# Performance work log

Measured on AMD Instinct MI355X. Metric: run time of the kernel, lower is better.

Reference implementation:

```python
import jax, jax.numpy as jnp
import numpy as np

LN_EPS = 1e-5


def setup_inputs() -> dict:
    key = jax.random.key(0)
    ks = jax.random.split(key, 8)
    B, S, N, D, H, E = 8, 32, 2048, 64, 128, 32768
    x_sequence = jax.random.normal(ks[0], (B, S, N, D), dtype=jnp.float32)
    edge_index = jax.random.randint(ks[1], (2, E), 0, N, dtype=jnp.int64)
    batch = jax.random.randint(ks[2], (B * N,), 0, B, dtype=jnp.int64)
    scale = 0.05
    Wz = jax.random.normal(ks[3], (D + H, H), dtype=jnp.float32) * scale
    Wr = jax.random.normal(ks[4], (D + H, H), dtype=jnp.float32) * scale
    Wc = jax.random.normal(ks[5], (D + H, H), dtype=jnp.float32) * scale
    bz = jnp.zeros((H,), jnp.float32)
    br = jnp.zeros((H,), jnp.float32)
    bc = jnp.zeros((H,), jnp.float32)
    ln_gamma = jnp.ones((H,), jnp.float32)
    ln_beta = jnp.zeros((H,), jnp.float32)
    return dict(x_sequence=x_sequence, edge_index=edge_index, batch=batch,
                Wz=Wz, bz=bz, Wr=Wr, br=br, Wc=Wc, bc=bc,
                ln_gamma=ln_gamma, ln_beta=ln_beta)


def reference(x_sequence, edge_index, batch, Wz, bz, Wr, br, Wc, bc, ln_gamma, ln_beta):
    B, S, N, D = x_sequence.shape
    H = Wz.shape[1]
    NT = B * N

    # Batch the per-graph edge list by offsetting node ids per batch element.
    offsets = jnp.arange(B, dtype=edge_index.dtype) * N
    src = (edge_index[0][None, :] + offsets[:, None]).reshape(-1)
    dst = (edge_index[1][None, :] + offsets[:, None]).reshape(-1)
    # GCNConv: add self loops, symmetric normalization D^-1/2 (A+I) D^-1/2.
    loops = jnp.arange(NT, dtype=edge_index.dtype)
    src = jnp.concatenate([src, loops])
    dst = jnp.concatenate([dst, loops])
    deg = jax.ops.segment_sum(jnp.ones_like(src, x_sequence.dtype), dst, num_segments=NT)
    dinv = jnp.where(deg > 0, jax.lax.rsqrt(jnp.maximum(deg, 1e-12)), 0.0)
    norm = dinv[src] * dinv[dst]  # [E_total]

    def gcn(x, W, b):
        h = x @ W                                   # [NT, H]
        msg = h[src] * norm[:, None]                # gather + scale
        return jax.ops.segment_sum(msg, dst, num_segments=NT) + b

    def layer_norm(h):
        mu = jnp.mean(h, axis=-1, keepdims=True)
        var = jnp.mean(jnp.square(h - mu), axis=-1, keepdims=True)
        return (h - mu) * jax.lax.rsqrt(var + LN_EPS) * ln_gamma + ln_beta

    def step(h_prev, x_t):
        # x_t: [NT, D], h_prev: [NT, H]
        xh = jnp.concatenate([x_t, h_prev], axis=1)
        z = jax.nn.sigmoid(gcn(xh, Wz, bz))
        r = jax.nn.sigmoid(gcn(xh, Wr, br))
        xrh = jnp.concatenate([x_t, r * h_prev], axis=1)
        cand = jnp.tanh(gcn(xrh, Wc, bc))
        h_new = layer_norm((1.0 - z) * h_prev + z * cand)
        return h_new, None

    xs = x_sequence.transpose(1, 0, 2, 3).reshape(S, NT, D)
    h0 = jnp.zeros((NT, H), x_sequence.dtype)
    h_final, _ = jax.lax.scan(step, h0, xs)

    # global_mean_pool over nodes per batch element (contiguous blocks of N).
    pooled = h_final.reshape(B, N, H).mean(axis=1)
    return pooled
```

## Files before the change

kernel.cpp:

```cpp
#include <hip/hip_runtime.h>
#include <math.h>

#define NB 8
#define NS 32
#define NN 2048
#define ND 64
#define NH 128
#define NE 32768
#define NT (NB*NN)
#define LN_EPS 1e-5f

typedef __attribute__((ext_vector_type(8))) short short8v;
typedef __attribute__((ext_vector_type(4))) float f32x4;
typedef __attribute__((ext_vector_type(4))) unsigned int u32x4;

static __device__ inline unsigned short f2bf(float f) {
  union { float f; unsigned int u; } v; v.f = f;
  unsigned int r = v.u + 0x7fffu + ((v.u >> 16) & 1u);
  return (unsigned short)(r >> 16);
}

static __device__ inline void bf8_to_f(const unsigned short* __restrict__ p, float* f) {
  u32x4 v = *(const u32x4*)p;
#pragma unroll
  for (int i = 0; i < 4; i++) {
    union { unsigned int u; float x; } lo, hi;
    lo.u = v[i] << 16; hi.u = v[i] & 0xFFFF0000u;
    f[2*i] = lo.x; f[2*i+1] = hi.x;
  }
}


__global__ void k_count(const int* __restrict__ dst, int* __restrict__ deg) {
  int e = blockIdx.x * blockDim.x + threadIdx.x;
  if (e < NE) atomicAdd(&deg[dst[e]], 1);
}

__global__ void k_scan(const int* __restrict__ deg, int* __restrict__ row_start,
                       float* __restrict__ dinv) {
  if (threadIdx.x == 0) {
    int acc = 0;
    for (int n = 0; n < NN; n++) { row_start[n] = acc; acc += deg[n]; }
    row_start[NN] = acc;
  }
  for (int n = threadIdx.x; n < NN; n += blockDim.x) {
    dinv[n] = rsqrtf((float)(deg[n] + 1));
  }
}

__global__ void k_scatter(const int* __restrict__ src, const int* __restrict__ dst,
                          const int* __restrict__ row_start, int* __restrict__ cursor,
                          int* __restrict__ csr_src) {
  int e = blockIdx.x * blockDim.x + threadIdx.x;
  if (e < NE) {
    int d = dst[e];
    int pos = atomicAdd(&cursor[d], 1);
    csr_src[row_start[d] + pos] = src[e];
  }
}


__global__ void k_wcvt(const float* __restrict__ Wz, const float* __restrict__ Wr,
                       const float* __restrict__ Wc,
                       unsigned short* __restrict__ Wt_zr, unsigned short* __restrict__ Wt_c) {
  int col = blockIdx.x;
  int k = threadIdx.x;
  float v = (col < 128) ? Wz[k * 128 + col] : Wr[k * 128 + (col - 128)];
  Wt_zr[(size_t)col * 192 + k] = f2bf(v);
  if (col < 128) Wt_c[(size_t)col * 192 + k] = f2bf(Wc[k * 128 + col]);
}


__global__ __launch_bounds__(256)
void k_xT(const float* __restrict__ x, unsigned short* __restrict__ xT) {
  int blk = blockIdx.x;
  int s = blk >> 9;
  int n0 = (blk & 511) * 4;
  int t = threadIdx.x;
  int b = t >> 5;
  int d2 = (t & 31) * 2;
#pragma unroll
  for (int i = 0; i < 4; i++) {
    int n = n0 + i;
    const float2 v = *(const float2*)(x + (((size_t)b * NS + s) * NN + n) * ND + d2);
    unsigned int p = ((unsigned int)f2bf(v.y) << 16) | f2bf(v.x);
    *(unsigned int*)(xT + (((size_t)s * NN + n) * NB + b) * ND + d2) = p;
  }
}


__global__ __launch_bounds__(256)
void k_aggX2(const unsigned short* __restrict__ xT, const int* __restrict__ row_start,
             const int* __restrict__ csr_src, const float* __restrict__ dinv,
             unsigned short* __restrict__ Xa) {
  int bid = blockIdx.x;
  int bs = (bid & 7) * 2048 + (bid >> 3);
  int rid = bs * 4 + (threadIdx.x >> 6);
  int lane = threadIdx.x & 63;
  int s = rid >> 11, n = rid & 2047;
  const unsigned short* xs = xT + (size_t)s * (NN * NB * ND);
  float dn = dinv[n];
  float acc[8], val[8];
  bf8_to_f(xs + (size_t)n * 512 + lane * 8, val);
#pragma unroll
  for (int i = 0; i < 8; i++) acc[i] = dn * val[i];
  int k0 = row_start[n], k1 = row_start[n + 1];
  for (int kb = k0; kb < k1; kb += 64) {
    int m = k1 - kb; if (m > 64) m = 64;
    int idx = 0; float wv = 0.f;
    if (lane < m) { idx = csr_src[kb + lane]; wv = dinv[idx]; }
    for (int k = 0; k < m; k++) {
      int sn = __shfl(idx, k, 64);
      float ww = __shfl(wv, k, 64);
      bf8_to_f(xs + (size_t)sn * 512 + lane * 8, val);
#pragma unroll
      for (int i = 0; i < 8; i++) acc[i] = fmaf(ww, val[i], acc[i]);
    }
  }
  unsigned int pk[4];
#pragma unroll
  for (int i = 0; i < 4; i++)
    pk[i] = ((unsigned int)f2bf(dn * acc[2*i+1]) << 16) | f2bf(dn * acc[2*i]);
  *(u32x4*)(Xa + (size_t)rid * 512 + lane * 8) = *(u32x4*)pk;
}


__global__ __launch_bounds__(256)
void k_zrF(const unsigned short* __restrict__ Xa, const unsigned short* __restrict__ hB,
           const float* __restrict__ h, const unsigned short* __restrict__ Wt,
           const int* __restrict__ row_start, const int* __restrict__ csr_src,
           const float* __restrict__ dinv,
           const float* __restrict__ bz, const float* __restrict__ br,
           float* __restrict__ z, unsigned short* __restrict__ rhB, int s) {
  __shared__ unsigned short ha[16 * 128];
  int tid = threadIdx.x;
  int lane = tid & 63;
  int w = tid >> 6;
  int n0 = blockIdx.x * 2;
  int j = w >> 1, half = w & 1;
  int n = n0 + j;
  float dn = dinv[n];
  float acc[8], val[8];
  int foff = half * 512 + lane * 8;
  bf8_to_f(hB + (size_t)n * (NB * NH) + foff, val);
#pragma unroll
  for (int i = 0; i < 8; i++) acc[i] = dn * val[i];
  int k0 = row_start[n], k1 = row_start[n + 1];
  for (int kb = k0; kb < k1; kb += 64) {
    int m = k1 - kb; if (m > 64) m = 64;
    int idx = 0; float wv = 0.f;
    if (lane < m) { idx = csr_src[kb + lane]; wv = dinv[idx]; }
    for (int k = 0; k < m; k++) {
      int sn = __shfl(idx, k, 64);
      float ww = __shfl(wv, k, 64);
      bf8_to_f(hB + (size_t)sn * (NB * NH) + foff, val);
#pragma unroll
      for (int i = 0; i < 8; i++) acc[i] = fmaf(ww, val[i], acc[i]);
    }
  }
  {
    int row = j * 8 + (foff >> 7);
    int f = foff & 127;
    unsigned int pk[4];
#pragma unroll
    for (int i = 0; i < 4; i++)
      pk[i] = ((unsigned int)f2bf(dn * acc[2*i+1]) << 16) | f2bf(dn * acc[2*i]);
    int byte = (row * 256 + f * 2) ^ ((row & 7) << 4);
    *(u32x4*)((char*)ha + byte) = *(u32x4*)pk;
  }
  __syncthreads();
  int ar = lane & 15;
  int koff = (lane >> 4) * 8;
  short8v afr[6];
  const unsigned short* xrow =
      Xa + (((size_t)s * NN + n0 + (ar >> 3)) * NB + (ar & 7)) * ND;
  afr[0] = *(const short8v*)(xrow + koff);
  afr[1] = *(const short8v*)(xrow + 32 + koff);
#pragma unroll
  for (int kb = 2; kb < 6; kb++) {
    int kk = (kb - 2) * 32 + koff;
    int byte = (ar * 256 + kk * 2) ^ ((ar & 7) << 4);
    afr[kb] = *(const short8v*)((char*)ha + byte);
  }
  f32x4 cacc[4];
#pragma unroll
  for (int ct = 0; ct < 4; ct++) cacc[ct] = (f32x4){0.f, 0.f, 0.f, 0.f};
#pragma unroll
  for (int ct = 0; ct < 4; ct++) {
    const unsigned short* wcol = Wt + (size_t)((w * 4 + ct) * 16 + (lane & 15)) * 192;
#pragma unroll
    for (int kb = 0; kb < 6; kb++) {
      short8v bfr = *(const short8v*)(wcol + kb * 32 + koff);
      cacc[ct] = __builtin_amdgcn_mfma_f32_16x16x32_bf16(afr[kb], bfr, cacc[ct], 0, 0, 0);
    }
  }
  int r0 = (lane >> 4) * 4;
#pragma unroll
  for (int ct = 0; ct < 4; ct++) {
    int col = (w * 4 + ct) * 16 + (lane & 15);
    int isz = (col < 128);
    int f = isz ? col : col - 128;
    float bias = isz ? bz[f] : br[f];
#pragma unroll
    for (int q = 0; q < 4; q++) {
      int r = r0 + q;
      size_t gidx = (((size_t)(n0 + (r >> 3))) * NB + (r & 7)) * NH + f;
      float g = cacc[ct][q] + bias;
      float sg = 1.f / (1.f + __expf(-g));
      if (isz) z[gidx] = sg;
      else rhB[gidx] = f2bf(sg * h[gidx]);
    }
  }
}


__global__ __launch_bounds__(256)
void k_cF(const unsigned short* __restrict__ Xa, const unsigned short* __restrict__ rhB,
          const float* __restrict__ z, const unsigned short* __restrict__ Wt,
          const int* __restrict__ row_start, const int* __restrict__ csr_src,
          const float* __restrict__ dinv, const float* __restrict__ bc,
          const float* __restrict__ gamma, const float* __restrict__ beta,
          float* __restrict__ h, unsigned short* __restrict__ hB, int s) {
  __shared__ unsigned short rha[16 * 128];
  __shared__ float lsum[4][16], lsq[4][16];
  int tid = threadIdx.x;
  int lane = tid & 63;
  int w = tid >> 6;
  int n0 = blockIdx.x * 2;
  int j = w >> 1, half = w & 1;
  int n = n0 + j;
  float dn = dinv[n];
  float acc[8], val[8];
  int foff = half * 512 + lane * 8;
  bf8_to_f(rhB + (size_t)n * (NB * NH) + foff, val);
#pragma unroll
  for (int i = 0; i < 8; i++) acc[i] = dn * val[i];
  int k0 = row_start[n], k1 = row_start[n + 1];
  for (int kb = k0; kb < k1; kb += 64) {
    int m = k1 - kb; if (m > 64) m = 64;
    int idx = 0; float wv = 0.f;
    if (lane < m) { idx = csr_src[kb + lane]; wv = dinv[idx]; }
    for (int k = 0; k < m; k++) {
      int sn = __shfl(idx, k, 64);
      float ww = __shfl(wv, k, 64);
      bf8_to_f(rhB + (size_t)sn * (NB * NH) + foff, val);
#pragma unroll
      for (int i = 0; i < 8; i++) acc[i] = fmaf(ww, val[i], acc[i]);
    }
  }
  {
    int row = j * 8 + (foff >> 7);
    int f = foff & 127;
    unsigned int pk[4];
#pragma unroll
    for (int i = 0; i < 4; i++)
      pk[i] = ((unsigned int)f2bf(dn * acc[2*i+1]) << 16) | f2bf(dn * acc[2*i]);
    int byte = (row * 256 + f * 2) ^ ((row & 7) << 4);
    *(u32x4*)((char*)rha + byte) = *(u32x4*)pk;
  }
  __syncthreads();
  int ar = lane & 15;
  int koff = (lane >> 4) * 8;
  short8v afr[6];
  const unsigned short* xrow =
      Xa + (((size_t)s * NN + n0 + (ar >> 3)) * NB + (ar & 7)) * ND;
  afr[0] = *(const short8v*)(xrow + koff);
  afr[1] = *(const short8v*)(xrow + 32 + koff);
#pragma unroll
  for (int kb = 2; kb < 6; kb++) {
    int kk = (kb - 2) * 32 + koff;
    int byte = (ar * 256 + kk * 2) ^ ((ar & 7) << 4);
    afr[kb] = *(const short8v*)((char*)rha + byte);
  }
  f32x4 cacc[2];
  cacc[0] = (f32x4){0.f, 0.f, 0.f, 0.f};
  cacc[1] = (f32x4){0.f, 0.f, 0.f, 0.f};
#pragma unroll
  for (int ct = 0; ct < 2; ct++) {
    const unsigned short* wcol = Wt + (size_t)((w * 2 + ct) * 16 + (lane & 15)) * 192;
#pragma unroll
    for (int kb = 0; kb < 6; kb++) {
      short8v bfr = *(const short8v*)(wcol + kb * 32 + koff);
      cacc[ct] = __builtin_amdgcn_mfma_f32_16x16x32_bf16(afr[kb], bfr, cacc[ct], 0, 0, 0);
    }
  }
  int r0 = (lane >> 4) * 4;
  float u[2][4];
  float psum[4] = {0.f, 0.f, 0.f, 0.f};
  float psq[4] = {0.f, 0.f, 0.f, 0.f};
#pragma unroll
  for (int ct = 0; ct < 2; ct++) {
    int col = (w * 2 + ct) * 16 + (lane & 15);
    float bcc = bc[col];
#pragma unroll
    for (int q = 0; q < 4; q++) {
      int r = r0 + q;
      size_t gidx = (((size_t)(n0 + (r >> 3))) * NB + (r & 7)) * NH + col;
      float gc = cacc[ct][q] + bcc;
      float ea = __expf(-2.f * fabsf(gc));
      float th = (1.f - ea) / (1.f + ea);
      float cand = copysignf(th, gc);
      float zv = z[gidx];
      float uu = (1.f - zv) * h[gidx] + zv * cand;
      u[ct][q] = uu;
      psum[q] += uu; psq[q] += uu * uu;
    }
  }
#pragma unroll
  for (int q = 0; q < 4; q++) {
    float s1 = psum[q], s2 = psq[q];
#pragma unroll
    for (int o = 1; o <= 8; o <<= 1) {
      s1 += __shfl_xor(s1, o, 64);
      s2 += __shfl_xor(s2, o, 64);
    }
    if ((lane & 15) == 0) {
      lsum[w][r0 + q] = s1; lsq[w][r0 + q] = s2;
    }
  }
  __syncthreads();
#pragma unroll
  for (int ct = 0; ct < 2; ct++) {
    int col = (w * 2 + ct) * 16 + (lane & 15);
    float g = gamma[col], bt = beta[col];
#pragma unroll
    for (int q = 0; q < 4; q++) {
      int r = r0 + q;
      float tot = lsum[0][r] + lsum[1][r] + lsum[2][r] + lsum[3][r];
      float totq = lsq[0][r] + lsq[1][r] + lsq[2][r] + lsq[3][r];
      float mu = tot * (1.f / NH);
      float var = totq * (1.f / NH) - mu * mu;
      float inv = rsqrtf(var + LN_EPS);
      float hv = (u[ct][q] - mu) * inv * g + bt;
      size_t gidx = (((size_t)(n0 + (r >> 3))) * NB + (r & 7)) * NH + col;
      h[gidx] = hv;
      hB[gidx] = f2bf(hv);
    }
  }
}


__global__ __launch_bounds__(128)
void k_pool(const float* __restrict__ h, float* __restrict__ out) {
  int b = blockIdx.x & 7;
  int c = blockIdx.x >> 3;
  int f = threadIdx.x;
  float acc = 0.f;
  for (int n = c * 128; n < c * 128 + 128; n++)
    acc += h[((size_t)n * NB + b) * NH + f];
  atomicAdd(&out[b * NH + f], acc * (1.f / NN));
}


extern "C" void kernel_launch(void* const* d_in, const int* in_sizes, int n_in,
                              void* d_out, int out_size, void* d_ws, size_t ws_size,
                              hipStream_t stream) {
  const float* x     = (const float*)d_in[0];
  const int*   ei    = (const int*)d_in[1];
  const float* Wz    = (const float*)d_in[3];
  const float* bz    = (const float*)d_in[4];
  const float* Wr    = (const float*)d_in[5];
  const float* br    = (const float*)d_in[6];
  const float* Wc    = (const float*)d_in[7];
  const float* bc    = (const float*)d_in[8];
  const float* gamma = (const float*)d_in[9];
  const float* beta  = (const float*)d_in[10];
  float* out = (float*)d_out;

  char* ws = (char*)d_ws;
  size_t off = 0;
  auto alloc = [&](size_t bytes) {
    void* p = ws + off;
    off = (off + bytes + 255) & ~(size_t)255;
    return p;
  };
  float* h  = (float*)alloc((size_t)NT * NH * 4);
  float* z  = (float*)alloc((size_t)NT * NH * 4);
  unsigned short* hB   = (unsigned short*)alloc((size_t)NT * NH * 2);
  unsigned short* rhB  = (unsigned short*)alloc((size_t)NT * NH * 2);
  unsigned short* xT   = (unsigned short*)alloc((size_t)NS * NN * NB * ND * 2);
  unsigned short* Xa   = (unsigned short*)alloc((size_t)NS * NN * NB * ND * 2);
  unsigned short* Wt_zr = (unsigned short*)alloc((size_t)256 * 192 * 2);
  unsigned short* Wt_c  = (unsigned short*)alloc((size_t)128 * 192 * 2);
  float* dinv = (float*)alloc(NN * 4);
  int* deg       = (int*)alloc(NN * 4);
  int* row_start = (int*)alloc((NN + 1) * 4);
  int* cursor    = (int*)alloc(NN * 4);
  int* csr_src   = (int*)alloc(NE * 4);

  const int* e_src = ei;
  const int* e_dst = ei + NE;

  hipMemsetAsync(h, 0, (size_t)NT * NH * 4, stream);
  hipMemsetAsync(hB, 0, (size_t)NT * NH * 2, stream);
  hipMemsetAsync(deg, 0, NN * 4, stream);
  hipMemsetAsync(cursor, 0, NN * 4, stream);
  hipMemsetAsync(d_out, 0, (size_t)NB * NH * 4, stream);

  k_count<<<NE / 256, 256, 0, stream>>>(e_dst, deg);
  k_scan<<<1, 256, 0, stream>>>(deg, row_start, dinv);
  k_scatter<<<NE / 256, 256, 0, stream>>>(e_src, e_dst, row_start, cursor, csr_src);
  k_wcvt<<<256, 192, 0, stream>>>(Wz, Wr, Wc, Wt_zr, Wt_c);
  k_xT<<<16384, 256, 0, stream>>>(x, xT);
  k_aggX2<<<16384, 256, 0, stream>>>(xT, row_start, csr_src, dinv, Xa);

  for (int s = 0; s < NS; s++) {
    k_zrF<<<NN / 2, 256, 0, stream>>>(Xa, hB, h, Wt_zr, row_start, csr_src, dinv,
                                      bz, br, z, rhB, s);
    k_cF<<<NN / 2, 256, 0, stream>>>(Xa, rhB, z, Wt_c, row_start, csr_src, dinv,
                                     bc, gamma, beta, h, hB, s);
  }
  k_pool<<<128, 128, 0, stream>>>(h, out);
}
```

Baseline: 1.783 ms.

## Drop fp32 hidden state, store z as fp16, double threads per step block

The fp32 hidden state and fp32 z buffers are removed. The recurrence now keeps only the bf16 hidden state, and z is stored in fp16, which roughly halves per-step global traffic. Both per-step kernels go from 256 to 512 threads, so each wave gathers 4 features instead of 8 and owns fewer MFMA output tiles, and the edge loops are unrolled by 4. The cost is precision: hidden state is carried in bf16 across all 32 steps, so rounding error can build up.

```diff
diff --git a/kernel.cpp b/kernel.cpp
--- a/kernel.cpp
+++ b/kernel.cpp
@@ -13,17 +13,31 @@
 typedef __attribute__((ext_vector_type(8))) short short8v;
 typedef __attribute__((ext_vector_type(4))) float f32x4;
 typedef __attribute__((ext_vector_type(4))) unsigned int u32x4;
+typedef __attribute__((ext_vector_type(2))) unsigned int u32x2;
 
 static __device__ inline unsigned short f2bf(float f) {
   union { float f; unsigned int u; } v; v.f = f;
   unsigned int r = v.u + 0x7fffu + ((v.u >> 16) & 1u);
   return (unsigned short)(r >> 16);
 }
+static __device__ inline float bf2f(unsigned short s) {
+  union { unsigned int u; float f; } v; v.u = ((unsigned int)s) << 16;
+  return v.f;
+}
 
 static __device__ inline void bf8_to_f(const unsigned short* __restrict__ p, float* f) {
   u32x4 v = *(const u32x4*)p;
 #pragma unroll
   for (int i = 0; i < 4; i++) {
+    union { unsigned int u; float x; } lo, hi;
+    lo.u = v[i] << 16; hi.u = v[i] & 0xFFFF0000u;
+    f[2*i] = lo.x; f[2*i+1] = hi.x;
+  }
+}
+static __device__ inline void bf4_to_f(const unsigned short* __restrict__ p, float* f) {
+  u32x2 v = *(const u32x2*)p;
+#pragma unroll
+  for (int i = 0; i < 2; i++) {
     union { unsigned int u; float x; } lo, hi;
     lo.u = v[i] << 16; hi.u = v[i] & 0xFFFF0000u;
     f[2*i] = lo.x; f[2*i+1] = hi.x;
@@ -109,6 +123,7 @@
     int m = k1 - kb; if (m > 64) m = 64;
     int idx = 0; float wv = 0.f;
     if (lane < m) { idx = csr_src[kb + lane]; wv = dinv[idx]; }
+#pragma unroll 4
     for (int k = 0; k < m; k++) {
       int sn = __shfl(idx, k, 64);
       float ww = __shfl(wv, k, 64);
@@ -125,48 +140,49 @@
 }
 
 
-__global__ __launch_bounds__(256)
+__global__ __launch_bounds__(512, 8)
 void k_zrF(const unsigned short* __restrict__ Xa, const unsigned short* __restrict__ hB,
-           const float* __restrict__ h, const unsigned short* __restrict__ Wt,
+           const unsigned short* __restrict__ Wt,
            const int* __restrict__ row_start, const int* __restrict__ csr_src,
            const float* __restrict__ dinv,
            const float* __restrict__ bz, const float* __restrict__ br,
-           float* __restrict__ z, unsigned short* __restrict__ rhB, int s) {
+           _Float16* __restrict__ zH, unsigned short* __restrict__ rhB, int s) {
   __shared__ unsigned short ha[16 * 128];
   int tid = threadIdx.x;
   int lane = tid & 63;
   int w = tid >> 6;
   int n0 = blockIdx.x * 2;
-  int j = w >> 1, half = w & 1;
+  int j = w >> 2, q = w & 3;
   int n = n0 + j;
   float dn = dinv[n];
-  float acc[8], val[8];
-  int foff = half * 512 + lane * 8;
-  bf8_to_f(hB + (size_t)n * (NB * NH) + foff, val);
-#pragma unroll
-  for (int i = 0; i < 8; i++) acc[i] = dn * val[i];
+  float acc[4], val[4];
+  int foff = q * 256 + lane * 4;
+  bf4_to_f(hB + (size_t)n * (NB * NH) + foff, val);
+#pragma unroll
+  for (int i = 0; i < 4; i++) acc[i] = dn * val[i];
   int k0 = row_start[n], k1 = row_start[n + 1];
   for (int kb = k0; kb < k1; kb += 64) {
     int m = k1 - kb; if (m > 64) m = 64;
     int idx = 0; float wv = 0.f;
     if (lane < m) { idx = csr_src[kb + lane]; wv = dinv[idx]; }
+#pragma unroll 4
     for (int k = 0; k < m; k++) {
       int sn = __shfl(idx, k, 64);
       float ww = __shfl(wv, k, 64);
-      bf8_to_f(hB + (size_t)sn * (NB * NH) + foff, val);
-#pragma unroll
-      for (int i = 0; i < 8; i++) acc[i] = fmaf(ww, val[i], acc[i]);
+      bf4_to_f(hB + (size_t)sn * (NB * NH) + foff, val);
+#pragma unroll
+      for (int i = 0; i < 4; i++) acc[i] = fmaf(ww, val[i], acc[i]);
     }
   }
   {
     int row = j * 8 + (foff >> 7);
-    int f = foff & 127;
-    unsigned int pk[4];
-#pragma unroll
-    for (int i = 0; i < 4; i++)
+    int fe = foff & 127;
+    unsigned int pk[2];
+#pragma unroll
+    for (int i = 0; i < 2; i++)
       pk[i] = ((unsigned int)f2bf(dn * acc[2*i+1]) << 16) | f2bf(dn * acc[2*i]);
-    int byte = (row * 256 + f * 2) ^ ((row & 7) << 4);
-    *(u32x4*)((char*)ha + byte) = *(u32x4*)pk;
+    int byte = (row * 256 + fe * 2) ^ ((row & 7) << 4);
+    *(u32x2*)((char*)ha + byte) = *(u32x2*)pk;
   }
   __syncthreads();
   int ar = lane & 15;
@@ -182,12 +198,12 @@
     int byte = (ar * 256 + kk * 2) ^ ((ar & 7) << 4);
     afr[kb] = *(const short8v*)((char*)ha + byte);
   }
-  f32x4 cacc[4];
-#pragma unroll
-  for (int ct = 0; ct < 4; ct++) cacc[ct] = (f32x4){0.f, 0.f, 0.f, 0.f};
-#pragma unroll
-  for (int ct = 0; ct < 4; ct++) {
-    const unsigned short* wcol = Wt + (size_t)((w * 4 + ct) * 16 + (lane & 15)) * 192;
+  f32x4 cacc[2];
+  cacc[0] = (f32x4){0.f, 0.f, 0.f, 0.f};
+  cacc[1] = (f32x4){0.f, 0.f, 0.f, 0.f};
+#pragma unroll
+  for (int ct = 0; ct < 2; ct++) {
+    const unsigned short* wcol = Wt + (size_t)((2 * w + ct) * 16 + (lane & 15)) * 192;
 #pragma unroll
     for (int kb = 0; kb < 6; kb++) {
       short8v bfr = *(const short8v*)(wcol + kb * 32 + koff);
@@ -196,67 +212,68 @@
   }
   int r0 = (lane >> 4) * 4;
 #pragma unroll
-  for (int ct = 0; ct < 4; ct++) {
-    int col = (w * 4 + ct) * 16 + (lane & 15);
+  for (int ct = 0; ct < 2; ct++) {
+    int col = (2 * w + ct) * 16 + (lane & 15);
     int isz = (col < 128);
     int f = isz ? col : col - 128;
     float bias = isz ? bz[f] : br[f];
 #pragma unroll
-    for (int q = 0; q < 4; q++) {
-      int r = r0 + q;
+    for (int qq = 0; qq < 4; qq++) {
+      int r = r0 + qq;
       size_t gidx = (((size_t)(n0 + (r >> 3))) * NB + (r & 7)) * NH + f;
-      float g = cacc[ct][q] + bias;
+      float g = cacc[ct][qq] + bias;
       float sg = 1.f / (1.f + __expf(-g));
-      if (isz) z[gidx] = sg;
-      else rhB[gidx] = f2bf(sg * h[gidx]);
-    }
-  }
-}
-
-
-__global__ __launch_bounds__(256)
+      if (isz) zH[gidx] = (_Float16)sg;
+      else rhB[gidx] = f2bf(sg * bf2f(hB[gidx]));
+    }
+  }
+}
+
+
+__global__ __launch_bounds__(512, 8)
 void k_cF(const unsigned short* __restrict__ Xa, const unsigned short* __restrict__ rhB,
-          const float* __restrict__ z, const unsigned short* __restrict__ Wt,
+          const _Float16* __restrict__ zH, const unsigned short* __restrict__ Wt,
           const int* __restrict__ row_start, const int* __restrict__ csr_src,
           const float* __restrict__ dinv, const float* __restrict__ bc,
           const float* __restrict__ gamma, const float* __restrict__ beta,
-          float* __restrict__ h, unsigned short* __restrict__ hB, int s) {
+          unsigned short* __restrict__ hB, int s) {
   __shared__ unsigned short rha[16 * 128];
-  __shared__ float lsum[4][16], lsq[4][16];
+  __shared__ float lsum[8][16], lsq[8][16];
   int tid = threadIdx.x;
   int lane = tid & 63;
   int w = tid >> 6;
   int n0 = blockIdx.x * 2;
-  int j = w >> 1, half = w & 1;
+  int j = w >> 2, q = w & 3;
   int n = n0 + j;
   float dn = dinv[n];
-  float acc[8], val[8];
-  int foff = half * 512 + lane * 8;
-  bf8_to_f(rhB + (size_t)n * (NB * NH) + foff, val);
-#pragma unroll
-  for (int i = 0; i < 8; i++) acc[i] = dn * val[i];
+  float acc[4], val[4];
+  int foff = q * 256 + lane * 4;
+  bf4_to_f(rhB + (size_t)n * (NB * NH) + foff, val);
+#pragma unroll
+  for (int i = 0; i < 4; i++) acc[i] = dn * val[i];
   int k0 = row_start[n], k1 = row_start[n + 1];
   for (int kb = k0; kb < k1; kb += 64) {
     int m = k1 - kb; if (m > 64) m = 64;
     int idx = 0; float wv = 0.f;
     if (lane < m) { idx = csr_src[kb + lane]; wv = dinv[idx]; }
+#pragma unroll 4
     for (int k = 0; k < m; k++) {
       int sn = __shfl(idx, k, 64);
       float ww = __shfl(wv, k, 64);
-      bf8_to_f(rhB + (size_t)sn * (NB * NH) + foff, val);
-#pragma unroll
-      for (int i = 0; i < 8; i++) acc[i] = fmaf(ww, val[i], acc[i]);
+      bf4_to_f(rhB + (size_t)sn * (NB * NH) + foff, val);
+#pragma unroll
+      for (int i = 0; i < 4; i++) acc[i] = fmaf(ww, val[i], acc[i]);
     }
   }
   {
     int row = j * 8 + (foff >> 7);
-    int f = foff & 127;
-    unsigned int pk[4];
-#pragma unroll
-    for (int i = 0; i < 4; i++)
+    int fe = foff & 127;
+    unsigned int pk[2];
+#pragma unroll
+    for (int i = 0; i < 2; i++)
       pk[i] = ((unsigned int)f2bf(dn * acc[2*i+1]) << 16) | f2bf(dn * acc[2*i]);
-    int byte = (row * 256 + f * 2) ^ ((row & 7) << 4);
-    *(u32x4*)((char*)rha + byte) = *(u32x4*)pk;
+    int byte = (row * 256 + fe * 2) ^ ((row & 7) << 4);
+    *(u32x2*)((char*)rha + byte) = *(u32x2*)pk;
   }
   __syncthreads();
   int ar = lane & 15;
@@ -272,82 +289,70 @@
     int byte = (ar * 256 + kk * 2) ^ ((ar & 7) << 4);
     afr[kb] = *(const short8v*)((char*)rha + byte);
   }
-  f32x4 cacc[2];
-  cacc[0] = (f32x4){0.f, 0.f, 0.f, 0.f};
-  cacc[1] = (f32x4){0.f, 0.f, 0.f, 0.f};
-#pragma unroll
-  for (int ct = 0; ct < 2; ct++) {
-    const unsigned short* wcol = Wt + (size_t)((w * 2 + ct) * 16 + (lane & 15)) * 192;
+  f32x4 cacc = {0.f, 0.f, 0.f, 0.f};
+  {
+    const unsigned short* wcol = Wt + (size_t)(w * 16 + (lane & 15)) * 192;
 #pragma unroll
     for (int kb = 0; kb < 6; kb++) {
       short8v bfr = *(const short8v*)(wcol + kb * 32 + koff);
-      cacc[ct] = __builtin_amdgcn_mfma_f32_16x16x32_bf16(afr[kb], bfr, cacc[ct], 0, 0, 0);
+      cacc = __builtin_amdgcn_mfma_f32_16x16x32_bf16(afr[kb], bfr, cacc, 0, 0, 0);
     }
   }
   int r0 = (lane >> 4) * 4;
-  float u[2][4];
-  float psum[4] = {0.f, 0.f, 0.f, 0.f};
-  float psq[4] = {0.f, 0.f, 0.f, 0.f};
-#pragma unroll
-  for (int ct = 0; ct < 2; ct++) {
-    int col = (w * 2 + ct) * 16 + (lane & 15);
-    float bcc = bc[col];
-#pragma unroll
-    for (int q = 0; q < 4; q++) {
-      int r = r0 + q;
-      size_t gidx = (((size_t)(n0 + (r >> 3))) * NB + (r & 7)) * NH + col;
-      float gc = cacc[ct][q] + bcc;
-      float ea = __expf(-2.f * fabsf(gc));
-      float th = (1.f - ea) / (1.f + ea);
-      float cand = copysignf(th, gc);
-      float zv = z[gidx];
-      float uu = (1.f - zv) * h[gidx] + zv * cand;
-      u[ct][q] = uu;
-      psum[q] += uu; psq[q] += uu * uu;
-    }
-  }
-#pragma unroll
-  for (int q = 0; q < 4; q++) {
-    float s1 = psum[q], s2 = psq[q];
+  int col = w * 16 + (lane & 15);
+  float u[4];
+  float bcc = bc[col];
+#pragma unroll
+  for (int qq = 0; qq < 4; qq++) {
+    int r = r0 + qq;
+    size_t gidx = (((size_t)(n0 + (r >> 3))) * NB + (r & 7)) * NH + col;
+    float gc = cacc[qq] + bcc;
+    float ea = __expf(-2.f * fabsf(gc));
+    float th = (1.f - ea) / (1.f + ea);
+    float cand = copysignf(th, gc);
+    float zv = (float)zH[gidx];
+    float uu = (1.f - zv) * bf2f(hB[gidx]) + zv * cand;
+    u[qq] = uu;
+  }
+#pragma unroll
+  for (int qq = 0; qq < 4; qq++) {
+    float s1 = u[qq], s2 = u[qq] * u[qq];
 #pragma unroll
     for (int o = 1; o <= 8; o <<= 1) {
       s1 += __shfl_xor(s1, o, 64);
       s2 += __shfl_xor(s2, o, 64);
     }
     if ((lane & 15) == 0) {
-      lsum[w][r0 + q] = s1; lsq[w][r0 + q] = s2;
+      lsum[w][r0 + qq] = s1; lsq[w][r0 + qq] = s2;
     }
   }
   __syncthreads();
-#pragma unroll
-  for (int ct = 0; ct < 2; ct++) {
-    int col = (w * 2 + ct) * 16 + (lane & 15);
-    float g = gamma[col], bt = beta[col];
-#pragma unroll
-    for (int q = 0; q < 4; q++) {
-      int r = r0 + q;
-      float tot = lsum[0][r] + lsum[1][r] + lsum[2][r] + lsum[3][r];
-      float totq = lsq[0][r] + lsq[1][r] + lsq[2][r] + lsq[3][r];
-      float mu = tot * (1.f / NH);
-      float var = totq * (1.f / NH) - mu * mu;
-      float inv = rsqrtf(var + LN_EPS);
-      float hv = (u[ct][q] - mu) * inv * g + bt;
-      size_t gidx = (((size_t)(n0 + (r >> 3))) * NB + (r & 7)) * NH + col;
-      h[gidx] = hv;
-      hB[gidx] = f2bf(hv);
-    }
+  float g = gamma[col], bt = beta[col];
+#pragma unroll
+  for (int qq = 0; qq < 4; qq++) {
+    int r = r0 + qq;
+    float tot = lsum[0][r] + lsum[1][r] + lsum[2][r] + lsum[3][r]
+              + lsum[4][r] + lsum[5][r] + lsum[6][r] + lsum[7][r];
+    float totq = lsq[0][r] + lsq[1][r] + lsq[2][r] + lsq[3][r]
+               + lsq[4][r] + lsq[5][r] + lsq[6][r] + lsq[7][r];
+    float mu = tot * (1.f / NH);
+    float var = totq * (1.f / NH) - mu * mu;
+    float inv = rsqrtf(var + LN_EPS);
+    float hv = (u[qq] - mu) * inv * g + bt;
+    size_t gidx = (((size_t)(n0 + (r >> 3))) * NB + (r & 7)) * NH + col;
+    hB[gidx] = f2bf(hv);
   }
 }
 
 
 __global__ __launch_bounds__(128)
-void k_pool(const float* __restrict__ h, float* __restrict__ out) {
+void k_pool(const unsigned short* __restrict__ hB, float* __restrict__ out) {
   int b = blockIdx.x & 7;
   int c = blockIdx.x >> 3;
   int f = threadIdx.x;
   float acc = 0.f;
   for (int n = c * 128; n < c * 128 + 128; n++)
-    acc += h[((size_t)n * NB + b) * NH + f];
+    acc += bf2f(hB[((size_t)n * NB + b) * NH + f]);
   atomicAdd(&out[b * NH + f], acc * (1.f / NN));
 }
 
@@ -374,10 +379,9 @@
     off = (off + bytes + 255) & ~(size_t)255;
     return p;
   };
-  float* h  = (float*)alloc((size_t)NT * NH * 4);
-  float* z  = (float*)alloc((size_t)NT * NH * 4);
   unsigned short* hB   = (unsigned short*)alloc((size_t)NT * NH * 2);
   unsigned short* rhB  = (unsigned short*)alloc((size_t)NT * NH * 2);
+  _Float16*       zH   = (_Float16*)alloc((size_t)NT * NH * 2);
   unsigned short* xT   = (unsigned short*)alloc((size_t)NS * NN * NB * ND * 2);
   unsigned short* Xa   = (unsigned short*)alloc((size_t)NS * NN * NB * ND * 2);
   unsigned short* Wt_zr = (unsigned short*)alloc((size_t)256 * 192 * 2);
@@ -391,7 +395,6 @@
   const int* e_src = ei;
   const int* e_dst = ei + NE;
 
-  hipMemsetAsync(h, 0, (size_t)NT * NH * 4, stream);
   hipMemsetAsync(hB, 0, (size_t)NT * NH * 2, stream);
   hipMemsetAsync(deg, 0, NN * 4, stream);
   hipMemsetAsync(cursor, 0, NN * 4, stream);
@@ -405,10 +408,10 @@
   k_aggX2<<<16384, 256, 0, stream>>>(xT, row_start, csr_src, dinv, Xa);
 
   for (int s = 0; s < NS; s++) {
-    k_zrF<<<NN / 2, 256, 0, stream>>>(Xa, hB, h, Wt_zr, row_start, csr_src, dinv,
-                                      bz, br, z, rhB, s);
-    k_cF<<<NN / 2, 256, 0, stream>>>(Xa, rhB, z, Wt_c, row_start, csr_src, dinv,
-                                     bc, gamma, beta, h, hB, s);
-  }
-  k_pool<<<128, 128, 0, stream>>>(h, out);
-}
+    k_zrF<<<NN / 2, 512, 0, stream>>>(Xa, hB, Wt_zr, row_start, csr_src, dinv,
+                                      bz, br, zH, rhB, s);
+    k_cF<<<NN / 2, 512, 0, stream>>>(Xa, rhB, zH, Wt_c, row_start, csr_src, dinv,
+                                     bc, gamma, beta, hB, s);
+  }
+  k_pool<<<128, 128, 0, stream>>>(hB, out);
+}
```

New measurement: 1.814 ms. About the same (+1.7%).

## Drop fp32 hidden state, store z in fp16, scalarize CSR neighbor loops

Applied to the files above, without the earlier changes.

Removes the fp32 copies of the hidden state and update gate, keeping h only in bf16 and z in fp16, which cuts global memory traffic in the per-step recurrent kernels. The gather loops now read the neighbor index and weight through scalar-uniform loads (readfirstlane bounds) instead of lane-distributed loads plus shuffles, and are unrolled. Carrying the recurrent state in bf16 across 32 steps lowers its precision, and the result may drift from the reference.

```diff
diff --git a/kernel.cpp b/kernel.cpp
--- a/kernel.cpp
+++ b/kernel.cpp
@@ -13,11 +13,16 @@
 typedef __attribute__((ext_vector_type(8))) short short8v;
 typedef __attribute__((ext_vector_type(4))) float f32x4;
 typedef __attribute__((ext_vector_type(4))) unsigned int u32x4;
+typedef __attribute__((ext_vector_type(2))) unsigned int u32x2;
 
 static __device__ inline unsigned short f2bf(float f) {
   union { float f; unsigned int u; } v; v.f = f;
   unsigned int r = v.u + 0x7fffu + ((v.u >> 16) & 1u);
   return (unsigned short)(r >> 16);
+}
+static __device__ inline float bf2f(unsigned short s) {
+  union { unsigned int u; float f; } v; v.u = ((unsigned int)s) << 16;
+  return v.f;
 }
 
 static __device__ inline void bf8_to_f(const unsigned short* __restrict__ p, float* f) {
@@ -97,25 +102,23 @@
   int bs = (bid & 7) * 2048 + (bid >> 3);
   int rid = bs * 4 + (threadIdx.x >> 6);
   int lane = threadIdx.x & 63;
-  int s = rid >> 11, n = rid & 2047;
+  int s = rid >> 11;
+  int n = __builtin_amdgcn_readfirstlane(rid & 2047);
   const unsigned short* xs = xT + (size_t)s * (NN * NB * ND);
   float dn = dinv[n];
   float acc[8], val[8];
   bf8_to_f(xs + (size_t)n * 512 + lane * 8, val);
 #pragma unroll
   for (int i = 0; i < 8; i++) acc[i] = dn * val[i];
-  int k0 = row_start[n], k1 = row_start[n + 1];
-  for (int kb = k0; kb < k1; kb += 64) {
-    int m = k1 - kb; if (m > 64) m = 64;
-    int idx = 0; float wv = 0.f;
-    if (lane < m) { idx = csr_src[kb + lane]; wv = dinv[idx]; }
-    for (int k = 0; k < m; k++) {
-      int sn = __shfl(idx, k, 64);
-      float ww = __shfl(wv, k, 64);
-      bf8_to_f(xs + (size_t)sn * 512 + lane * 8, val);
-#pragma unroll
-      for (int i = 0; i < 8; i++) acc[i] = fmaf(ww, val[i], acc[i]);
-    }
+  int k0 = __builtin_amdgcn_readfirstlane(row_start[n]);
+  int k1 = __builtin_amdgcn_readfirstlane(row_start[n + 1]);
+#pragma unroll 4
+  for (int k = k0; k < k1; k++) {
+    int sn = csr_src[k];
+    float ww = dinv[sn];
+    bf8_to_f(xs + (size_t)sn * 512 + lane * 8, val);
+#pragma unroll
+    for (int i = 0; i < 8; i++) acc[i] = fmaf(ww, val[i], acc[i]);
   }
   unsigned int pk[4];
 #pragma unroll
@@ -127,45 +130,42 @@
 
 __global__ __launch_bounds__(256)
 void k_zrF(const unsigned short* __restrict__ Xa, const unsigned short* __restrict__ hB,
-           const float* __restrict__ h, const unsigned short* __restrict__ Wt,
+           const unsigned short* __restrict__ Wt,
            const int* __restrict__ row_start, const int* __restrict__ csr_src,
            const float* __restrict__ dinv,
            const float* __restrict__ bz, const float* __restrict__ br,
-           float* __restrict__ z, unsigned short* __restrict__ rhB, int s) {
+           _Float16* __restrict__ zH, unsigned short* __restrict__ rhB, int s) {
   __shared__ unsigned short ha[16 * 128];
   int tid = threadIdx.x;
   int lane = tid & 63;
   int w = tid >> 6;
   int n0 = blockIdx.x * 2;
   int j = w >> 1, half = w & 1;
-  int n = n0 + j;
+  int n = __builtin_amdgcn_readfirstlane(n0 + j);
   float dn = dinv[n];
   float acc[8], val[8];
   int foff = half * 512 + lane * 8;
   bf8_to_f(hB + (size_t)n * (NB * NH) + foff, val);
 #pragma unroll
   for (int i = 0; i < 8; i++) acc[i] = dn * val[i];
-  int k0 = row_start[n], k1 = row_start[n + 1];
-  for (int kb = k0; kb < k1; kb += 64) {
-    int m = k1 - kb; if (m > 64) m = 64;
-    int idx = 0; float wv = 0.f;
-    if (lane < m) { idx = csr_src[kb + lane]; wv = dinv[idx]; }
-    for (int k = 0; k < m; k++) {
-      int sn = __shfl(idx, k, 64);
-      float ww = __shfl(wv, k, 64);
-      bf8_to_f(hB + (size_t)sn * (NB * NH) + foff, val);
-#pragma unroll
-      for (int i = 0; i < 8; i++) acc[i] = fmaf(ww, val[i], acc[i]);
-    }
+  int k0 = __builtin_amdgcn_readfirstlane(row_start[n]);
+  int k1 = __builtin_amdgcn_readfirstlane(row_start[n + 1]);
+#pragma unroll 4
+  for (int k = k0; k < k1; k++) {
+    int sn = csr_src[k];
+    float ww = dinv[sn];
+    bf8_to_f(hB + (size_t)sn * (NB * NH) + foff, val);
+#pragma unroll
+    for (int i = 0; i < 8; i++) acc[i] = fmaf(ww, val[i], acc[i]);
   }
   {
     int row = j * 8 + (foff >> 7);
-    int f = foff & 127;
+    int fe = foff & 127;
     unsigned int pk[4];
 #pragma unroll
     for (int i = 0; i < 4; i++)
       pk[i] = ((unsigned int)f2bf(dn * acc[2*i+1]) << 16) | f2bf(dn * acc[2*i]);
-    int byte = (row * 256 + f * 2) ^ ((row & 7) << 4);
+    int byte = (row * 256 + fe * 2) ^ ((row & 7) << 4);
     *(u32x4*)((char*)ha + byte) = *(u32x4*)pk;
   }
   __syncthreads();
@@ -202,13 +202,13 @@
     int f = isz ? col : col - 128;
     float bias = isz ? bz[f] : br[f];
 #pragma unroll
-    for (int q = 0; q < 4; q++) {
-      int r = r0 + q;
+    for (int qq = 0; qq < 4; qq++) {
+      int r = r0 + qq;
       size_t gidx = (((size_t)(n0 + (r >> 3))) * NB + (r & 7)) * NH + f;
-      float g = cacc[ct][q] + bias;
+      float g = cacc[ct][qq] + bias;
       float sg = 1.f / (1.f + __expf(-g));
-      if (isz) z[gidx] = sg;
-      else rhB[gidx] = f2bf(sg * h[gidx]);
+      if (isz) zH[gidx] = (_Float16)sg;
+      else rhB[gidx] = f2bf(sg * bf2f(hB[gidx]));
     }
   }
 }
@@ -216,11 +216,11 @@
 
 __global__ __launch_bounds__(256)
 void k_cF(const unsigned short* __restrict__ Xa, const unsigned short* __restrict__ rhB,
-          const float* __restrict__ z, const unsigned short* __restrict__ Wt,
+          const _Float16* __restrict__ zH, const unsigned short* __restrict__ Wt,
           const int* __restrict__ row_start, const int* __restrict__ csr_src,
           const float* __restrict__ dinv, const float* __restrict__ bc,
           const float* __restrict__ gamma, const float* __restrict__ beta,
-          float* __restrict__ h, unsigned short* __restrict__ hB, int s) {
+          unsigned short* __restrict__ hB, int s) {
   __shared__ unsigned short rha[16 * 128];
   __shared__ float lsum[4][16], lsq[4][16];
   int tid = threadIdx.x;
@@ -228,34 +228,31 @@
   int w = tid >> 6;
   int n0 = blockIdx.x * 2;
   int j = w >> 1, half = w & 1;
-  int n = n0 + j;
+  int n = __builtin_amdgcn_readfirstlane(n0 + j);
   float dn = dinv[n];
   float acc[8], val[8];
   int foff = half * 512 + lane * 8;
   bf8_to_f(rhB + (size_t)n * (NB * NH) + foff, val);
 #pragma unroll
   for (int i = 0; i < 8; i++) acc[i] = dn * val[i];
-  int k0 = row_start[n], k1 = row_start[n + 1];
-  for (int kb = k0; kb < k1; kb += 64) {
-    int m = k1 - kb; if (m > 64) m = 64;
-    int idx = 0; float wv = 0.f;
-    if (lane < m) { idx = csr_src[kb + lane]; wv = dinv[idx]; }
-    for (int k = 0; k < m; k++) {
-      int sn = __shfl(idx, k, 64);
-      float ww = __shfl(wv, k, 64);
-      bf8_to_f(rhB + (size_t)sn * (NB * NH) + foff, val);
-#pragma unroll
-      for (int i = 0; i < 8; i++) acc[i] = fmaf(ww, val[i], acc[i]);
-    }
+  int k0 = __builtin_amdgcn_readfirstlane(row_start[n]);
+  int k1 = __builtin_amdgcn_readfirstlane(row_start[n + 1]);
+#pragma unroll 4
+  for (int k = k0; k < k1; k++) {
+    int sn = csr_src[k];
+    float ww = dinv[sn];
+    bf8_to_f(rhB + (size_t)sn * (NB * NH) + foff, val);
+#pragma unroll
+    for (int i = 0; i < 8; i++) acc[i] = fmaf(ww, val[i], acc[i]);
   }
   {
     int row = j * 8 + (foff >> 7);
-    int f = foff & 127;
+    int fe = foff & 127;
     unsigned int pk[4];
 #pragma unroll
     for (int i = 0; i < 4; i++)
       pk[i] = ((unsigned int)f2bf(dn * acc[2*i+1]) << 16) | f2bf(dn * acc[2*i]);
-    int byte = (row * 256 + f * 2) ^ ((row & 7) << 4);
+    int byte = (row * 256 + fe * 2) ^ ((row & 7) << 4);
     *(u32x4*)((char*)rha + byte) = *(u32x4*)pk;
   }
   __syncthreads();
@@ -293,29 +290,29 @@
     int col = (w * 2 + ct) * 16 + (lane & 15);
     float bcc = bc[col];
 #pragma unroll
-    for (int q = 0; q < 4; q++) {
-      int r = r0 + q;
+    for (int qq = 0; qq < 4; qq++) {
+      int r = r0 + qq;
       size_t gidx = (((size_t)(n0 + (r >> 3))) * NB + (r & 7)) * NH + col;
-      float gc = cacc[ct][q] + bcc;
+      float gc = cacc[ct][qq] + bcc;
       float ea = __expf(-2.f * fabsf(gc));
       float th = (1.f - ea) / (1.f + ea);
       float cand = copysignf(th, gc);
-      float zv = z[gidx];
-      float uu = (1.f - zv) * h[gidx] + zv * cand;
-      u[ct][q] = uu;
-      psum[q] += uu; psq[q] += uu * uu;
-    }
-  }
-#pragma unroll
-  for (int q = 0; q < 4; q++) {
-    float s1 = psum[q], s2 = psq[q];
+      float zv = (float)zH[gidx];
+      float uu = (1.f - zv) * bf2f(hB[gidx]) + zv * cand;
+      u[ct][qq] = uu;
+      psum[qq] += uu; psq[qq] += uu * uu;
+    }
+  }
+#pragma unroll
+  for (int qq = 0; qq < 4; qq++) {
+    float s1 = psum[qq], s2 = psq[qq];
 #pragma unroll
     for (int o = 1; o <= 8; o <<= 1) {
       s1 += __shfl_xor(s1, o, 64);
       s2 += __shfl_xor(s2, o, 64);
     }
     if ((lane & 15) == 0) {
-      lsum[w][r0 + q] = s1; lsq[w][r0 + q] = s2;
+      lsum[w][r0 + qq] = s1; lsq[w][r0 + qq] = s2;
     }
   }
   __syncthreads();
@@ -324,16 +321,15 @@
     int col = (w * 2 + ct) * 16 + (lane & 15);
     float g = gamma[col], bt = beta[col];
 #pragma unroll
-    for (int q = 0; q < 4; q++) {
-      int r = r0 + q;
+    for (int qq = 0; qq < 4; qq++) {
+      int r = r0 + qq;
       float tot = lsum[0][r] + lsum[1][r] + lsum[2][r] + lsum[3][r];
       float totq = lsq[0][r] + lsq[1][r] + lsq[2][r] + lsq[3][r];
       float mu = tot * (1.f / NH);
       float var = totq * (1.f / NH) - mu * mu;
       float inv = rsqrtf(var + LN_EPS);
-      float hv = (u[ct][q] - mu) * inv * g + bt;
+      float hv = (u[ct][qq] - mu) * inv * g + bt;
       size_t gidx = (((size_t)(n0 + (r >> 3))) * NB + (r & 7)) * NH + col;
-      h[gidx] = hv;
       hB[gidx] = f2bf(hv);
     }
   }
@@ -341,13 +337,13 @@
 
 
 __global__ __launch_bounds__(128)
-void k_pool(const float* __restrict__ h, float* __restrict__ out) {
+void k_pool(const unsigned short* __restrict__ hB, float* __restrict__ out) {
   int b = blockIdx.x & 7;
   int c = blockIdx.x >> 3;
   int f = threadIdx.x;
   float acc = 0.f;
   for (int n = c * 128; n < c * 128 + 128; n++)
-    acc += h[((size_t)n * NB + b) * NH + f];
+    acc += bf2f(hB[((size_t)n * NB + b) * NH + f]);
   atomicAdd(&out[b * NH + f], acc * (1.f / NN));
 }
 
@@ -374,10 +370,9 @@
     off = (off + bytes + 255) & ~(size_t)255;
     return p;
   };
-  float* h  = (float*)alloc((size_t)NT * NH * 4);
-  float* z  = (float*)alloc((size_t)NT * NH * 4);
   unsigned short* hB   = (unsigned short*)alloc((size_t)NT * NH * 2);
   unsigned short* rhB  = (unsigned short*)alloc((size_t)NT * NH * 2);
+  _Float16*       zH   = (_Float16*)alloc((size_t)NT * NH * 2);
   unsigned short* xT   = (unsigned short*)alloc((size_t)NS * NN * NB * ND * 2);
   unsigned short* Xa   = (unsigned short*)alloc((size_t)NS * NN * NB * ND * 2);
   unsigned short* Wt_zr = (unsigned short*)alloc((size_t)256 * 192 * 2);
@@ -391,7 +386,6 @@
   const int* e_src = ei;
   const int* e_dst = ei + NE;
 
-  hipMemsetAsync(h, 0, (size_t)NT * NH * 4, stream);
   hipMemsetAsync(hB, 0, (size_t)NT * NH * 2, stream);
   hipMemsetAsync(deg, 0, NN * 4, stream);
   hipMemsetAsync(cursor, 0, NN * 4, stream);
@@ -405,10 +399,10 @@
   k_aggX2<<<16384, 256, 0, stream>>>(xT, row_start, csr_src, dinv, Xa);
 
   for (int s = 0; s < NS; s++) {
-    k_zrF<<<NN / 2, 256, 0, stream>>>(Xa, hB, h, Wt_zr, row_start, csr_src, dinv,
-                                      bz, br, z, rhB, s);
-    k_cF<<<NN / 2, 256, 0, stream>>>(Xa, rhB, z, Wt_c, row_start, csr_src, dinv,
-                                     bc, gamma, beta, h, hB, s);
-  }
-  k_pool<<<128, 128, 0, stream>>>(h, out);
-}
+    k_zrF<<<NN / 2, 256, 0, stream>>>(Xa, hB, Wt_zr, row_start, csr_src, dinv,
+                                      bz, br, zH, rhB, s);
+    k_cF<<<NN / 2, 256, 0, stream>>>(Xa, rhB, zH, Wt_c, row_start, csr_src, dinv,
+                                     bc, gamma, beta, hB, s);
+  }
+  k_pool<<<128, 128, 0, stream>>>(hB, out);
+}
```

After: 1.451 ms. 1.23x faster.
